# Kernel tuning notes

Hardware: AMD Instinct MI355X
Metric: run time of the kernel (lower is better)

## Reference

```python
import jax, jax.numpy as jnp
import numpy as np

E = 1024
H = 16
DFF = 4 * E
EPS = 1e-5


def layer_norm(x, scale, bias):
    mu = jnp.mean(x, axis=-1, keepdims=True)
    var = jnp.var(x, axis=-1, keepdims=True)
    return (x - mu) * jax.lax.rsqrt(var + EPS) * scale + bias


def setup_inputs() -> dict:
    key = jax.random.key(0)
    ks = jax.random.split(key, 12)
    N, L = 2, 2048
    x = jax.random.normal(ks[0], (N, L, E), dtype=jnp.float32)
    attn_mask = jax.random.randint(ks[1], (N, H, L, L), 0, 2) == 1
    s = 0.02
    return {
        "x": x,
        "attn_mask": attn_mask,
        "ln1_s": jnp.ones((E,), jnp.float32),
        "ln1_b": jnp.zeros((E,), jnp.float32),
        "Wqkv": jax.random.normal(ks[2], (E, 3 * E), jnp.float32) * s,
        "bqkv": jnp.zeros((3 * E,), jnp.float32),
        "Wo": jax.random.normal(ks[3], (E, E), jnp.float32) * s,
        "bo": jnp.zeros((E,), jnp.float32),
        "ln2_s": jnp.ones((E,), jnp.float32),
        "ln2_b": jnp.zeros((E,), jnp.float32),
        "lnf_s": jnp.ones((E,), jnp.float32),
        "lnf_b": jnp.zeros((E,), jnp.float32),
        "W1": jax.random.normal(ks[4], (E, DFF), jnp.float32) * s,
        "b1": jnp.zeros((DFF,), jnp.float32),
        "W2": jax.random.normal(ks[5], (DFF, E), jnp.float32) * s,
        "b2": jnp.zeros((E,), jnp.float32),
    }


def reference(x, attn_mask, ln1_s, ln1_b, Wqkv, bqkv, Wo, bo,
              ln2_s, ln2_b, lnf_s, lnf_b, W1, b1, W2, b2):
    N, L, _ = x.shape
    D = E // H
    # --- self attention (pre-norm) ---
    h = layer_norm(x, ln1_s, ln1_b)
    qkv = h @ Wqkv + bqkv                      # [N,L,3E]
    q, k, v = jnp.split(qkv, 3, axis=-1)
    q = q.reshape(N, L, H, D)
    k = k.reshape(N, L, H, D)
    v = v.reshape(N, L, H, D)
    a = jnp.einsum('nqhd,nkhd->nhqk', q, k) * (D ** -0.5)  # [N,H,L,L]
    a = jnp.where(attn_mask, -jnp.inf, a)
    a = jax.nn.softmax(a, axis=-1)
    o = jnp.einsum('nhqk,nkhd->nqhd', a, v).reshape(N, L, E)
    o = o @ Wo + bo
    x = x + o
    # --- feedforward (norm_2 then FF's internal LN) ---
    h = layer_norm(x, ln2_s, ln2_b)
    h = layer_norm(h, lnf_s, lnf_b)
    h = jax.nn.gelu(h @ W1 + b1, approximate=False) @ W2 + b2
    return x + h
```

## Files before the change

### kernel.cpp

```cpp
#include <hip/hip_runtime.h>
#include <math.h>

#define E_DIM 1024
#define H_HEADS 16
#define D_HEAD 64
#define DFF_DIM 4096
#define L_SEQ 2048
#define N_BATCH 2
#define T_TOK (N_BATCH * L_SEQ)

typedef __attribute__((ext_vector_type(8))) __bf16 bf16x8;
typedef __attribute__((ext_vector_type(4))) float f32x4;

__device__ __forceinline__ unsigned short f2bf(float f) {
  union { float f; unsigned int u; } v; v.f = f;
  unsigned int r = v.u + 0x7fffu + ((v.u >> 16) & 1u);
  return (unsigned short)(r >> 16);
}

__device__ __forceinline__ void gld16(const void* g, void* l) {
  __builtin_amdgcn_global_load_lds(
      (const __attribute__((address_space(1))) unsigned int*)g,
      (__attribute__((address_space(3))) unsigned int*)l, 16, 0, 0);
}

__global__ __launch_bounds__(256) void convert_transpose(
    const float* __restrict__ in, unsigned short* __restrict__ out, int K, int N) {
  __shared__ float tile[32][33];
  int n0 = blockIdx.x * 32, k0 = blockIdx.y * 32;
  int tx = threadIdx.x & 31, ty = threadIdx.x >> 5;
#pragma unroll
  for (int i = 0; i < 32; i += 8)
    tile[ty + i][tx] = in[(size_t)(k0 + ty + i) * N + n0 + tx];
  __syncthreads();
#pragma unroll
  for (int i = 0; i < 32; i += 8)
    out[(size_t)(n0 + ty + i) * K + k0 + tx] = f2bf(tile[tx][ty + i]);
}

__device__ __forceinline__ void block_reduce2(float& a, float& b, float* sm, int tid) {
#pragma unroll
  for (int off = 32; off > 0; off >>= 1) {
    a += __shfl_down(a, off);
    b += __shfl_down(b, off);
  }
  int wid = tid >> 6;
  if ((tid & 63) == 0) { sm[wid * 2] = a; sm[wid * 2 + 1] = b; }
  __syncthreads();
  a = sm[0] + sm[2] + sm[4] + sm[6];
  b = sm[1] + sm[3] + sm[5] + sm[7];
}

__global__ __launch_bounds__(256) void ln_kernel(
    const float* __restrict__ x, const float* __restrict__ s,
    const float* __restrict__ b, unsigned short* __restrict__ out) {
  int row = blockIdx.x, tid = threadIdx.x;
  __shared__ float sm[8];
  float4 v = ((const float4*)(x + (size_t)row * E_DIM))[tid];
  float sum = v.x + v.y + v.z + v.w;
  float sq = v.x * v.x + v.y * v.y + v.z * v.z + v.w * v.w;
  block_reduce2(sum, sq, sm, tid);
  float mu = sum * (1.0f / E_DIM);
  float var = sq * (1.0f / E_DIM) - mu * mu;
  float rs = rsqrtf(var + 1e-5f);
  float4 sv = ((const float4*)s)[tid];
  float4 bv = ((const float4*)b)[tid];
  ushort4 o4;
  o4.x = f2bf((v.x - mu) * rs * sv.x + bv.x);
  o4.y = f2bf((v.y - mu) * rs * sv.y + bv.y);
  o4.z = f2bf((v.z - mu) * rs * sv.z + bv.z);
  o4.w = f2bf((v.w - mu) * rs * sv.w + bv.w);
  ((ushort4*)(out + (size_t)row * E_DIM))[tid] = o4;
}

__global__ __launch_bounds__(256) void ln2_fused_kernel(
    const float* __restrict__ p0, const float* __restrict__ p1,
    const float* __restrict__ x, const float* __restrict__ bo,
    const float* __restrict__ s2, const float* __restrict__ b2,
    const float* __restrict__ sf, const float* __restrict__ bf_,
    float* __restrict__ x2, unsigned short* __restrict__ out) {
  int row = blockIdx.x, tid = threadIdx.x;
  __shared__ float sm[8];
  float4 a0 = ((const float4*)(p0 + (size_t)row * E_DIM))[tid];
  float4 a1 = ((const float4*)(p1 + (size_t)row * E_DIM))[tid];
  float4 xv = ((const float4*)(x + (size_t)row * E_DIM))[tid];
  float4 bov = ((const float4*)bo)[tid];
  float4 v;
  v.x = a0.x + a1.x + xv.x + bov.x;
  v.y = a0.y + a1.y + xv.y + bov.y;
  v.z = a0.z + a1.z + xv.z + bov.z;
  v.w = a0.w + a1.w + xv.w + bov.w;
  ((float4*)(x2 + (size_t)row * E_DIM))[tid] = v;
  float sum = v.x + v.y + v.z + v.w;
  float sq = v.x * v.x + v.y * v.y + v.z * v.z + v.w * v.w;
  block_reduce2(sum, sq, sm, tid);
  float mu = sum * (1.0f / E_DIM);
  float rs = rsqrtf(sq * (1.0f / E_DIM) - mu * mu + 1e-5f);
  float4 s2v = ((const float4*)s2)[tid];
  float4 b2v = ((const float4*)b2)[tid];
  float y0 = (v.x - mu) * rs * s2v.x + b2v.x;
  float y1 = (v.y - mu) * rs * s2v.y + b2v.y;
  float y2 = (v.z - mu) * rs * s2v.z + b2v.z;
  float y3 = (v.w - mu) * rs * s2v.w + b2v.w;
  float sum2 = y0 + y1 + y2 + y3;
  float sq2 = y0 * y0 + y1 * y1 + y2 * y2 + y3 * y3;
  __syncthreads();
  block_reduce2(sum2, sq2, sm, tid);
  float mu2 = sum2 * (1.0f / E_DIM);
  float rs2 = rsqrtf(sq2 * (1.0f / E_DIM) - mu2 * mu2 + 1e-5f);
  float4 sfv = ((const float4*)sf)[tid];
  float4 bfv = ((const float4*)bf_)[tid];
  ushort4 o4;
  o4.x = f2bf((y0 - mu2) * rs2 * sfv.x + bfv.x);
  o4.y = f2bf((y1 - mu2) * rs2 * sfv.y + bfv.y);
  o4.z = f2bf((y2 - mu2) * rs2 * sfv.z + bfv.z);
  o4.w = f2bf((y3 - mu2) * rs2 * sfv.w + bfv.w);
  ((ushort4*)(out + (size_t)row * E_DIM))[tid] = o4;
}

__global__ __launch_bounds__(256) void add4_kernel(
    const float* __restrict__ p0, const float* __restrict__ p1,
    const float* __restrict__ p2, const float* __restrict__ p3,
    const float* __restrict__ resid, const float* __restrict__ bias,
    float* __restrict__ out) {
  int row = blockIdx.x, tid = threadIdx.x;
  size_t base = (size_t)row * E_DIM;
  float4 a0 = ((const float4*)(p0 + base))[tid];
  float4 a1 = ((const float4*)(p1 + base))[tid];
  float4 a2 = ((const float4*)(p2 + base))[tid];
  float4 a3 = ((const float4*)(p3 + base))[tid];
  float4 rv = ((const float4*)(resid + base))[tid];
  float4 bv = ((const float4*)bias)[tid];
  float4 o;
  o.x = a0.x + a1.x + a2.x + a3.x + rv.x + bv.x;
  o.y = a0.y + a1.y + a2.y + a3.y + rv.y + bv.y;
  o.z = a0.z + a1.z + a2.z + a3.z + rv.z + bv.z;
  o.w = a0.w + a1.w + a2.w + a3.w + rv.w + bv.w;
  ((float4*)(out + base))[tid] = o;
}

template <int EPI>
__global__ __launch_bounds__(256) void gemm_bt(
    const unsigned short* __restrict__ A, const unsigned short* __restrict__ Bt,
    const float* __restrict__ bias, void* __restrict__ outp,
    int M, int N, int K, int Ks) {
  __shared__ unsigned short As[128 * 32];
  __shared__ unsigned short Bs[128 * 32];
  int tid = threadIdx.x;
  int lane = tid & 63, wave = tid >> 6;
  int m0 = blockIdx.y * 128, n0 = blockIdx.x * 128;
  int kz = blockIdx.z * Ks;
  int wm = (wave & 1) * 64, wn = (wave >> 1) * 64;
  int lm = lane & 15, lq = lane >> 4;
  int srow = wave * 32 + (lane >> 2);
  int scol = (lane & 3) * 8;
  const unsigned short* Ag = A + (size_t)(m0 + srow) * K + scol;
  const unsigned short* Bg = Bt + (size_t)(n0 + srow) * K + scol;
  unsigned short* AsW = As + wave * 1024;
  unsigned short* BsW = Bs + wave * 1024;
  f32x4 acc[4][4] = {};
  for (int k0 = kz; k0 < kz + Ks; k0 += 32) {
    __syncthreads();
    gld16(Ag + k0, AsW);
    gld16(Ag + (size_t)16 * K + k0, AsW + 512);
    gld16(Bg + k0, BsW);
    gld16(Bg + (size_t)16 * K + k0, BsW + 512);
    __syncthreads();
    bf16x8 a[4], b[4];
#pragma unroll
    for (int i = 0; i < 4; i++)
      a[i] = *(const bf16x8*)(As + (wm + i * 16 + lm) * 32 + lq * 8);
#pragma unroll
    for (int j = 0; j < 4; j++)
      b[j] = *(const bf16x8*)(Bs + (wn + j * 16 + lm) * 32 + lq * 8);
#pragma unroll
    for (int i = 0; i < 4; i++)
#pragma unroll
      for (int j = 0; j < 4; j++)
        acc[i][j] = __builtin_amdgcn_mfma_f32_16x16x32_bf16(a[i], b[j], acc[i][j], 0, 0, 0);
  }
  float* pout = (EPI == 3) ? ((float*)outp + (size_t)blockIdx.z * M * N) : nullptr;
#pragma unroll
  for (int i = 0; i < 4; i++)
#pragma unroll
    for (int j = 0; j < 4; j++) {
      int row = m0 + wm + i * 16 + lq * 4;
      int col = n0 + wn + j * 16 + lm;
      float bcol = (EPI == 3) ? 0.0f : bias[col];
#pragma unroll
      for (int r = 0; r < 4; r++) {
        float v = acc[i][j][r] + bcol;
        size_t idx = (size_t)(row + r) * N + col;
        if (EPI == 0) {
          ((unsigned short*)outp)[idx] = f2bf(v);
        } else if (EPI == 1) {
          float g = 0.5f * v * (1.0f + erff(v * 0.70710678118f));
          ((unsigned short*)outp)[idx] = f2bf(g);
        } else {
          pout[idx] = v;
        }
      }
    }
}

__global__ __launch_bounds__(256) void attn_kernel(
    const unsigned short* __restrict__ qkv, const int* __restrict__ mask,
    unsigned short* __restrict__ o) {
  const int bq = blockIdx.x;
  const int nh = blockIdx.y;
  const int h = nh & 15;
  const int tid = threadIdx.x, lane = tid & 63, wave = tid >> 6;
  const int lm = lane & 15, lq = lane >> 4;

  __shared__ unsigned short Ks[64 * 72];
  __shared__ unsigned short Vt[64 * 72];
  __shared__ unsigned short Ps[4][16 * 72];

  const int q_base = bq * 64;
  const int tok0 = (nh >> 4) * L_SEQ;
  const int qoff = h * 64, koff = E_DIM + h * 64, voff = 2 * E_DIM + h * 64;
  const int* mbase = mask + (size_t)nh * L_SEQ * L_SEQ;

  bf16x8 qf[2];
  {
    int t = tok0 + q_base + wave * 16 + lm;
    const unsigned short* qr = qkv + (size_t)t * (3 * E_DIM) + qoff + lq * 8;
    qf[0] = *(const bf16x8*)(qr);
    qf[1] = *(const bf16x8*)(qr + 32);
  }

  float m_run[4], l_run[4];
  f32x4 oacc[4] = {};
#pragma unroll
  for (int r = 0; r < 4; r++) { m_run[r] = -1e30f; l_run[r] = 0.0f; }

  for (int kt = 0; kt < L_SEQ / 64; kt++) {
    const int k_base = kt * 64;
    __syncthreads();
    {
      int row = tid >> 3, chunk = tid & 7;
#pragma unroll
      for (int it = 0; it < 2; it++) {
        int key = row + it * 32;
        int t = tok0 + k_base + key;
        uint4 kv = *(const uint4*)(qkv + (size_t)t * (3 * E_DIM) + koff + chunk * 8);
        *(uint4*)(Ks + key * 72 + chunk * 8) = kv;
        uint4 vv = *(const uint4*)(qkv + (size_t)t * (3 * E_DIM) + voff + chunk * 8);
        const unsigned short* vs = (const unsigned short*)&vv;
        int kcol = key ^ (chunk << 3);
#pragma unroll
        for (int jj = 0; jj < 8; jj++)
          Vt[(chunk * 8 + jj) * 72 + kcol] = vs[jj];
      }
    }
    __syncthreads();

    f32x4 s[4];
#pragma unroll
    for (int nt = 0; nt < 4; nt++) {
      bf16x8 kb0 = *(const bf16x8*)(Ks + (nt * 16 + lm) * 72 + lq * 8);
      bf16x8 kb1 = *(const bf16x8*)(Ks + (nt * 16 + lm) * 72 + 32 + lq * 8);
      f32x4 acc = {};
      acc = __builtin_amdgcn_mfma_f32_16x16x32_bf16(qf[0], kb0, acc, 0, 0, 0);
      acc = __builtin_amdgcn_mfma_f32_16x16x32_bf16(qf[1], kb1, acc, 0, 0, 0);
      s[nt] = acc;
    }
    const int qrow = q_base + wave * 16 + lq * 4;
#pragma unroll
    for (int nt = 0; nt < 4; nt++) {
      int kcol = k_base + nt * 16 + lm;
#pragma unroll
      for (int r = 0; r < 4; r++) {
        float v = s[nt][r] * 0.125f;
        int mval = mbase[(size_t)(qrow + r) * L_SEQ + kcol];
        s[nt][r] = mval ? -1e30f : v;
      }
    }
    float alpha[4], rsum[4];
#pragma unroll
    for (int r = 0; r < 4; r++) {
      float v = fmaxf(fmaxf(s[0][r], s[1][r]), fmaxf(s[2][r], s[3][r]));
#pragma unroll
      for (int mo = 1; mo < 16; mo <<= 1) v = fmaxf(v, __shfl_xor(v, mo));
      float mn = fmaxf(m_run[r], v);
      alpha[r] = __expf(m_run[r] - mn);
      m_run[r] = mn;
      rsum[r] = 0.0f;
    }
    unsigned short* pw = Ps[wave];
#pragma unroll
    for (int nt = 0; nt < 4; nt++)
#pragma unroll
      for (int r = 0; r < 4; r++) {
        float p = __expf(s[nt][r] - m_run[r]);
        rsum[r] += p;
        pw[(lq * 4 + r) * 72 + nt * 16 + lm] = f2bf(p);
      }
#pragma unroll
    for (int r = 0; r < 4; r++) {
      float v = rsum[r];
#pragma unroll
      for (int mo = 1; mo < 16; mo <<= 1) v += __shfl_xor(v, mo);
      l_run[r] = l_run[r] * alpha[r] + v;
    }
#pragma unroll
    for (int j = 0; j < 4; j++)
#pragma unroll
      for (int r = 0; r < 4; r++) oacc[j][r] *= alpha[r];
    __syncthreads();

#pragma unroll
    for (int c = 0; c < 2; c++) {
      bf16x8 pa = *(const bf16x8*)(pw + lm * 72 + c * 32 + lq * 8);
#pragma unroll
      for (int j = 0; j < 4; j++) {
        int d = j * 16 + lm;
        int kblk = (c * 4 + lq) ^ ((d >> 3) & 7);
        bf16x8 vb = *(const bf16x8*)(Vt + d * 72 + kblk * 8);
        oacc[j] = __builtin_amdgcn_mfma_f32_16x16x32_bf16(pa, vb, oacc[j], 0, 0, 0);
      }
    }
  }
  const int qrow = q_base + wave * 16 + lq * 4;
#pragma unroll
  for (int r = 0; r < 4; r++) {
    float inv_l = 1.0f / l_run[r];
    int t = tok0 + qrow + r;
#pragma unroll
    for (int j = 0; j < 4; j++)
      o[(size_t)t * E_DIM + h * 64 + j * 16 + lm] = f2bf(oacc[j][r] * inv_l);
  }
}

extern "C" void kernel_launch(void* const* d_in, const int* in_sizes, int n_in,
                              void* d_out, int out_size, void* d_ws, size_t ws_size,
                              hipStream_t stream) {
  const float* x = (const float*)d_in[0];
  const int* mask = (const int*)d_in[1];
  const float* ln1_s = (const float*)d_in[2];
  const float* ln1_b = (const float*)d_in[3];
  const float* Wqkv = (const float*)d_in[4];
  const float* bqkv = (const float*)d_in[5];
  const float* Wo = (const float*)d_in[6];
  const float* bo = (const float*)d_in[7];
  const float* ln2_s = (const float*)d_in[8];
  const float* ln2_b = (const float*)d_in[9];
  const float* lnf_s = (const float*)d_in[10];
  const float* lnf_b = (const float*)d_in[11];
  const float* W1 = (const float*)d_in[12];
  const float* b1 = (const float*)d_in[13];
  const float* W2 = (const float*)d_in[14];
  const float* b2 = (const float*)d_in[15];

  size_t off = 0;
  auto alloc = [&](size_t bytes) {
    void* p = (char*)d_ws + off;
    off += (bytes + 255) & ~(size_t)255;
    return p;
  };
  unsigned short* WqkvT = (unsigned short*)alloc((size_t)3072 * 1024 * 2);
  unsigned short* WoT = (unsigned short*)alloc((size_t)1024 * 1024 * 2);
  unsigned short* W1T = (unsigned short*)alloc((size_t)4096 * 1024 * 2);
  unsigned short* W2T = (unsigned short*)alloc((size_t)1024 * 4096 * 2);
  unsigned short* h1 = (unsigned short*)alloc((size_t)T_TOK * E_DIM * 2);
  unsigned short* qkvb = (unsigned short*)alloc((size_t)T_TOK * 3 * E_DIM * 2);
  unsigned short* ob = (unsigned short*)alloc((size_t)T_TOK * E_DIM * 2);
  float* x2 = (float*)alloc((size_t)T_TOK * E_DIM * 4);
  unsigned short* h2 = (unsigned short*)alloc((size_t)T_TOK * E_DIM * 2);
  unsigned short* g1 = (unsigned short*)alloc((size_t)T_TOK * DFF_DIM * 2);
  float* part = (float*)alloc((size_t)4 * T_TOK * E_DIM * 4);
  const size_t PSTRIDE = (size_t)T_TOK * E_DIM;

  convert_transpose<<<dim3(3072 / 32, 1024 / 32), 256, 0, stream>>>(Wqkv, WqkvT, 1024, 3072);
  convert_transpose<<<dim3(1024 / 32, 1024 / 32), 256, 0, stream>>>(Wo, WoT, 1024, 1024);
  convert_transpose<<<dim3(4096 / 32, 1024 / 32), 256, 0, stream>>>(W1, W1T, 1024, 4096);
  convert_transpose<<<dim3(1024 / 32, 4096 / 32), 256, 0, stream>>>(W2, W2T, 4096, 1024);
  ln_kernel<<<T_TOK, 256, 0, stream>>>(x, ln1_s, ln1_b, h1);
  gemm_bt<0><<<dim3(3072 / 128, T_TOK / 128, 1), 256, 0, stream>>>(
      h1, WqkvT, bqkv, qkvb, T_TOK, 3072, 1024, 1024);
  attn_kernel<<<dim3(L_SEQ / 64, N_BATCH * H_HEADS), 256, 0, stream>>>(qkvb, mask, ob);
  gemm_bt<3><<<dim3(1024 / 128, T_TOK / 128, 2), 256, 0, stream>>>(
      ob, WoT, nullptr, part, T_TOK, 1024, 1024, 512);
  ln2_fused_kernel<<<T_TOK, 256, 0, stream>>>(
      part, part + PSTRIDE, x, bo, ln2_s, ln2_b, lnf_s, lnf_b, x2, h2);
  gemm_bt<1><<<dim3(DFF_DIM / 128, T_TOK / 128, 1), 256, 0, stream>>>(
      h2, W1T, b1, g1, T_TOK, DFF_DIM, 1024, 1024);
  gemm_bt<3><<<dim3(1024 / 128, T_TOK / 128, 4), 256, 0, stream>>>(
      g1, W2T, nullptr, part, T_TOK, 1024, 4096, 1024);
  add4_kernel<<<T_TOK, 256, 0, stream>>>(
      part, part + PSTRIDE, part + 2 * PSTRIDE, part + 3 * PSTRIDE,
      x2, b2, (float*)d_out);

  (void)in_sizes; (void)n_in; (void)out_size; (void)ws_size;
}
```

Baseline: 1.056 ms.

## Pack attention mask into bitwords and swizzle GEMM block order

Adds a pre-pass that turns the int32 attention mask into 64-bit ballot bitmasks, so the attention kernel loads one word per row per key tile instead of scattered 4-byte ints. This replaces a large, poorly coalesced mask read inside attention with one streaming read plus a tiny bitmask. The GEMM also remaps block indices into 8 groups to improve L2 locality. The extra pack kernel still reads the full 512MB mask once per call.

```diff
diff --git a/kernel.cpp b/kernel.cpp
--- a/kernel.cpp
+++ b/kernel.cpp
@@ -22,6 +22,19 @@
   __builtin_amdgcn_global_load_lds(
       (const __attribute__((address_space(1))) unsigned int*)g,
       (__attribute__((address_space(3))) unsigned int*)l, 16, 0, 0);
+}
+
+__global__ __launch_bounds__(256) void mask_pack(
+    const int* __restrict__ mask, unsigned long long* __restrict__ bits,
+    long long nwords) {
+  int lane = threadIdx.x & 63;
+  long long w = (long long)blockIdx.x * 4 + (threadIdx.x >> 6);
+  long long stride = (long long)gridDim.x * 4;
+  for (; w < nwords; w += stride) {
+    int m = mask[w * 64 + lane];
+    unsigned long long b = __ballot(m != 0);
+    if (lane == 0) bits[w] = b;
+  }
 }
 
 __global__ __launch_bounds__(256) void convert_transpose(
@@ -148,7 +161,12 @@
   __shared__ unsigned short Bs[128 * 32];
   int tid = threadIdx.x;
   int lane = tid & 63, wave = tid >> 6;
-  int m0 = blockIdx.y * 128, n0 = blockIdx.x * 128;
+  int gx = gridDim.x;
+  int orig = blockIdx.y * gx + blockIdx.x;
+  int cpx = (gx * gridDim.y) >> 3;
+  int swz = (orig & 7) * cpx + (orig >> 3);
+  int bx = swz % gx, by = swz / gx;
+  int m0 = by * 128, n0 = bx * 128;
   int kz = blockIdx.z * Ks;
   int wm = (wave & 1) * 64, wn = (wave >> 1) * 64;
   int lm = lane & 15, lq = lane >> 4;
@@ -204,7 +222,8 @@
 }
 
 __global__ __launch_bounds__(256) void attn_kernel(
-    const unsigned short* __restrict__ qkv, const int* __restrict__ mask,
+    const unsigned short* __restrict__ qkv,
+    const unsigned long long* __restrict__ mbits,
     unsigned short* __restrict__ o) {
   const int bq = blockIdx.x;
   const int nh = blockIdx.y;
@@ -219,7 +238,8 @@
   const int q_base = bq * 64;
   const int tok0 = (nh >> 4) * L_SEQ;
   const int qoff = h * 64, koff = E_DIM + h * 64, voff = 2 * E_DIM + h * 64;
-  const int* mbase = mask + (size_t)nh * L_SEQ * L_SEQ;
+  const unsigned long long* mb =
+      mbits + (size_t)nh * L_SEQ * (L_SEQ / 64);
 
   bf16x8 qf[2];
   {
@@ -233,6 +253,8 @@
   f32x4 oacc[4] = {};
 #pragma unroll
   for (int r = 0; r < 4; r++) { m_run[r] = -1e30f; l_run[r] = 0.0f; }
+
+  const int qrow = q_base + wave * 16 + lq * 4;
 
   for (int kt = 0; kt < L_SEQ / 64; kt++) {
     const int k_base = kt * 64;
@@ -255,6 +277,14 @@
     }
     __syncthreads();
 
+    unsigned int mlo[4], mhi[4];
+#pragma unroll
+    for (int r = 0; r < 4; r++) {
+      unsigned long long mw = mb[(size_t)(qrow + r) * (L_SEQ / 64) + kt];
+      mlo[r] = (unsigned int)mw;
+      mhi[r] = (unsigned int)(mw >> 32);
+    }
+
     f32x4 s[4];
 #pragma unroll
     for (int nt = 0; nt < 4; nt++) {
@@ -265,15 +295,14 @@
       acc = __builtin_amdgcn_mfma_f32_16x16x32_bf16(qf[1], kb1, acc, 0, 0, 0);
       s[nt] = acc;
     }
-    const int qrow = q_base + wave * 16 + lq * 4;
 #pragma unroll
     for (int nt = 0; nt < 4; nt++) {
-      int kcol = k_base + nt * 16 + lm;
+      int sh = (nt & 1) * 16 + lm;
 #pragma unroll
       for (int r = 0; r < 4; r++) {
         float v = s[nt][r] * 0.125f;
-        int mval = mbase[(size_t)(qrow + r) * L_SEQ + kcol];
-        s[nt][r] = mval ? -1e30f : v;
+        unsigned int bit = ((nt < 2 ? mlo[r] : mhi[r]) >> sh) & 1u;
+        s[nt][r] = bit ? -1e30f : v;
       }
     }
     float alpha[4], rsum[4];
@@ -321,7 +350,6 @@
       }
     }
   }
-  const int qrow = q_base + wave * 16 + lq * 4;
 #pragma unroll
   for (int r = 0; r < 4; r++) {
     float inv_l = 1.0f / l_run[r];
@@ -369,8 +397,12 @@
   unsigned short* h2 = (unsigned short*)alloc((size_t)T_TOK * E_DIM * 2);
   unsigned short* g1 = (unsigned short*)alloc((size_t)T_TOK * DFF_DIM * 2);
   float* part = (float*)alloc((size_t)4 * T_TOK * E_DIM * 4);
+  const long long MWORDS =
+      (long long)N_BATCH * H_HEADS * L_SEQ * (L_SEQ / 64);
+  unsigned long long* mbits = (unsigned long long*)alloc((size_t)MWORDS * 8);
   const size_t PSTRIDE = (size_t)T_TOK * E_DIM;
 
+  mask_pack<<<4096, 256, 0, stream>>>(mask, mbits, MWORDS);
   convert_transpose<<<dim3(3072 / 32, 1024 / 32), 256, 0, stream>>>(Wqkv, WqkvT, 1024, 3072);
   convert_transpose<<<dim3(1024 / 32, 1024 / 32), 256, 0, stream>>>(Wo, WoT, 1024, 1024);
   convert_transpose<<<dim3(4096 / 32, 1024 / 32), 256, 0, stream>>>(W1, W1T, 1024, 4096);
@@ -378,7 +410,7 @@
   ln_kernel<<<T_TOK, 256, 0, stream>>>(x, ln1_s, ln1_b, h1);
   gemm_bt<0><<<dim3(3072 / 128, T_TOK / 128, 1), 256, 0, stream>>>(
       h1, WqkvT, bqkv, qkvb, T_TOK, 3072, 1024, 1024);
-  attn_kernel<<<dim3(L_SEQ / 64, N_BATCH * H_HEADS), 256, 0, stream>>>(qkvb, mask, ob);
+  attn_kernel<<<dim3(L_SEQ / 64, N_BATCH * H_HEADS), 256, 0, stream>>>(qkvb, mbits, ob);
   gemm_bt<3><<<dim3(1024 / 128, T_TOK / 128, 2), 256, 0, stream>>>(
       ob, WoT, nullptr, part, T_TOK, 1024, 1024, 512);
   ln2_fused_kernel<<<T_TOK, 256, 0, stream>>>(
```

Measured after the change: 1.158 ms. +9.6%, slower.

## Double-buffer K/V tiles and prefetch mask into registers in attention kernel

Applied to the files above, without the earlier changes.

The attention kernel now double-buffers the K and V^T shared-memory tiles. The next tile's K/V and mask values are loaded into registers during the softmax of the current tile and written to the alternate buffer after the PV MFMAs, which removes one block barrier per iteration. A per-wave lgkmcnt wait replaces the barrier before reading the wave-private P tile, and s_setprio raises priority around the MFMA sections. The cost is more register pressure (16 mask ints plus K/V staging) and twice the LDS, which may reduce occupancy.

```diff
diff --git a/kernel.cpp b/kernel.cpp
--- a/kernel.cpp
+++ b/kernel.cpp
@@ -212,8 +212,8 @@
   const int tid = threadIdx.x, lane = tid & 63, wave = tid >> 6;
   const int lm = lane & 15, lq = lane >> 4;
 
-  __shared__ unsigned short Ks[64 * 72];
-  __shared__ unsigned short Vt[64 * 72];
+  __shared__ unsigned short Ksm[2][64 * 72];
+  __shared__ unsigned short Vtm[2][64 * 72];
   __shared__ unsigned short Ps[4][16 * 72];
 
   const int q_base = bq * 64;
@@ -229,53 +229,82 @@
     qf[1] = *(const bf16x8*)(qr + 32);
   }
 
+  const int qrow = q_base + wave * 16 + lq * 4;
+  const int srow = tid >> 3, schunk = tid & 7;
+  const size_t TS = 3 * E_DIM;
+  const unsigned short* kg = qkv + (size_t)(tok0 + srow) * TS + koff + schunk * 8;
+  const unsigned short* vg = qkv + (size_t)(tok0 + srow) * TS + voff + schunk * 8;
+
+  uint4 kreg[2], vreg[2];
+  int mreg[16];
+
+  auto load_kv = [&](int kt) {
+#pragma unroll
+    for (int it = 0; it < 2; it++) {
+      size_t toff = (size_t)(kt * 64 + it * 32) * TS;
+      kreg[it] = *(const uint4*)(kg + toff);
+      vreg[it] = *(const uint4*)(vg + toff);
+    }
+  };
+  auto load_m = [&](int kt) {
+#pragma unroll
+    for (int nt = 0; nt < 4; nt++)
+#pragma unroll
+      for (int r = 0; r < 4; r++)
+        mreg[nt * 4 + r] =
+            mbase[(size_t)(qrow + r) * L_SEQ + kt * 64 + nt * 16 + lm];
+  };
+  auto store_kv = [&](int buf) {
+#pragma unroll
+    for (int it = 0; it < 2; it++) {
+      int key = srow + it * 32;
+      *(uint4*)(Ksm[buf] + key * 72 + schunk * 8) = kreg[it];
+      const unsigned short* vs = (const unsigned short*)&vreg[it];
+      int kcol = key ^ (schunk << 3);
+#pragma unroll
+      for (int jj = 0; jj < 8; jj++)
+        Vtm[buf][(schunk * 8 + jj) * 72 + kcol] = vs[jj];
+    }
+  };
+
   float m_run[4], l_run[4];
   f32x4 oacc[4] = {};
 #pragma unroll
   for (int r = 0; r < 4; r++) { m_run[r] = -1e30f; l_run[r] = 0.0f; }
 
-  for (int kt = 0; kt < L_SEQ / 64; kt++) {
-    const int k_base = kt * 64;
-    __syncthreads();
-    {
-      int row = tid >> 3, chunk = tid & 7;
-#pragma unroll
-      for (int it = 0; it < 2; it++) {
-        int key = row + it * 32;
-        int t = tok0 + k_base + key;
-        uint4 kv = *(const uint4*)(qkv + (size_t)t * (3 * E_DIM) + koff + chunk * 8);
-        *(uint4*)(Ks + key * 72 + chunk * 8) = kv;
-        uint4 vv = *(const uint4*)(qkv + (size_t)t * (3 * E_DIM) + voff + chunk * 8);
-        const unsigned short* vs = (const unsigned short*)&vv;
-        int kcol = key ^ (chunk << 3);
-#pragma unroll
-        for (int jj = 0; jj < 8; jj++)
-          Vt[(chunk * 8 + jj) * 72 + kcol] = vs[jj];
-      }
-    }
-    __syncthreads();
-
+  load_kv(0);
+  load_m(0);
+  store_kv(0);
+  __syncthreads();
+
+  int cur = 0;
+  const int NT = L_SEQ / 64;
+  for (int kt = 0; kt < NT; kt++) {
     f32x4 s[4];
+    __builtin_amdgcn_s_setprio(1);
 #pragma unroll
     for (int nt = 0; nt < 4; nt++) {
-      bf16x8 kb0 = *(const bf16x8*)(Ks + (nt * 16 + lm) * 72 + lq * 8);
-      bf16x8 kb1 = *(const bf16x8*)(Ks + (nt * 16 + lm) * 72 + 32 + lq * 8);
+      bf16x8 kb0 = *(const bf16x8*)(Ksm[cur] + (nt * 16 + lm) * 72 + lq * 8);
+      bf16x8 kb1 = *(const bf16x8*)(Ksm[cur] + (nt * 16 + lm) * 72 + 32 + lq * 8);
       f32x4 acc = {};
       acc = __builtin_amdgcn_mfma_f32_16x16x32_bf16(qf[0], kb0, acc, 0, 0, 0);
       acc = __builtin_amdgcn_mfma_f32_16x16x32_bf16(qf[1], kb1, acc, 0, 0, 0);
       s[nt] = acc;
     }
-    const int qrow = q_base + wave * 16 + lq * 4;
-#pragma unroll
-    for (int nt = 0; nt < 4; nt++) {
-      int kcol = k_base + nt * 16 + lm;
+    __builtin_amdgcn_s_setprio(0);
+
+#pragma unroll
+    for (int nt = 0; nt < 4; nt++)
 #pragma unroll
       for (int r = 0; r < 4; r++) {
         float v = s[nt][r] * 0.125f;
-        int mval = mbase[(size_t)(qrow + r) * L_SEQ + kcol];
-        s[nt][r] = mval ? -1e30f : v;
+        s[nt][r] = mreg[nt * 4 + r] ? -1e30f : v;
       }
-    }
+
+    int ktn = (kt + 1 < NT) ? kt + 1 : kt;
+    load_kv(ktn);
+    load_m(ktn);
+
     float alpha[4], rsum[4];
 #pragma unroll
     for (int r = 0; r < 4; r++) {
@@ -307,8 +336,11 @@
     for (int j = 0; j < 4; j++)
 #pragma unroll
       for (int r = 0; r < 4; r++) oacc[j][r] *= alpha[r];
-    __syncthreads();
-
+
+    asm volatile("s_waitcnt lgkmcnt(0)" ::: "memory");
+    __builtin_amdgcn_sched_barrier(0);
+
+    __builtin_amdgcn_s_setprio(1);
 #pragma unroll
     for (int c = 0; c < 2; c++) {
       bf16x8 pa = *(const bf16x8*)(pw + lm * 72 + c * 32 + lq * 8);
@@ -316,12 +348,17 @@
       for (int j = 0; j < 4; j++) {
         int d = j * 16 + lm;
         int kblk = (c * 4 + lq) ^ ((d >> 3) & 7);
-        bf16x8 vb = *(const bf16x8*)(Vt + d * 72 + kblk * 8);
+        bf16x8 vb = *(const bf16x8*)(Vtm[cur] + d * 72 + kblk * 8);
         oacc[j] = __builtin_amdgcn_mfma_f32_16x16x32_bf16(pa, vb, oacc[j], 0, 0, 0);
       }
     }
+    __builtin_amdgcn_s_setprio(0);
+
+    store_kv(cur ^ 1);
+    __syncthreads();
+    cur ^= 1;
   }
-  const int qrow = q_base + wave * 16 + lq * 4;
+
 #pragma unroll
   for (int r = 0; r < 4; r++) {
     float inv_l = 1.0f / l_run[r];
```

After: 1.060 ms. No clear change (+0.4%).
